# Kernel tuning notes

Measured on AMD Instinct MI355X. Metric: run time of the kernel, lower is better.

Reference implementation:

```python
import jax, jax.numpy as jnp
import numpy as np

B, D, N, H = 2, 512, 2048, 8
DK = D // H
EPS = 1e-5


def conv1x1(x, w, b):
    # kernel-size-1 Conv1d == channel-mixing GEMM: (o,i) x (b,i,n) -> (b,o,n)
    return jnp.einsum('oi,bin->bon', w, x) + b[None, :, None]


def setup_inputs() -> dict:
    key = jax.random.key(0)
    ks = jax.random.split(key, 20)
    s = 0.02
    return {
        'init_query': jax.random.normal(ks[0], (B, D, N), jnp.float32),
        'key_t': jax.random.normal(ks[1], (B, D, N), jnp.float32),
        'value': jax.random.normal(ks[2], (B, D, N), jnp.float32),
        'mask': jax.random.randint(ks[3], (B, 1, N, N), 0, 2, jnp.int32),
        'Wq': jax.random.normal(ks[4], (D, D), jnp.float32) * s,
        'bq': jax.random.normal(ks[5], (D,), jnp.float32) * s,
        'Wk': jax.random.normal(ks[6], (D, D), jnp.float32) * s,
        'bk': jax.random.normal(ks[7], (D,), jnp.float32) * s,
        'Wv': jax.random.normal(ks[8], (D, D), jnp.float32) * s,
        'bv': jax.random.normal(ks[9], (D,), jnp.float32) * s,
        'Wm': jax.random.normal(ks[10], (D, D), jnp.float32) * s,
        'bm': jax.random.normal(ks[11], (D,), jnp.float32) * s,
        'W1': jax.random.normal(ks[12], (2 * D, 2 * D), jnp.float32) * s,
        'b1': jax.random.normal(ks[13], (2 * D,), jnp.float32) * s,
        'gamma': jnp.ones((2 * D,), jnp.float32),
        'beta': jnp.zeros((2 * D,), jnp.float32),
        'rmean': jax.random.normal(ks[14], (2 * D,), jnp.float32) * s,
        'rvar': jnp.abs(jax.random.normal(ks[15], (2 * D,), jnp.float32)) * 0.1 + 0.5,
        'W2': jax.random.normal(ks[16], (D, 2 * D), jnp.float32) * s,
        'b2': jnp.zeros((D,), jnp.float32),  # nn.init.constant_(bias, 0.0)
    }


def reference(init_query, key_t, value, mask, Wq, bq, Wk, bk, Wv, bv, Wm, bm,
              W1, b1, gamma, beta, rmean, rvar, W2, b2):
    # projections, split channels into (d_k, n_heads) exactly like torch .view
    q = conv1x1(init_query, Wq, bq).reshape(B, DK, H, N)
    k = conv1x1(key_t, Wk, bk).reshape(B, DK, H, N)
    v = conv1x1(value, Wv, bv).reshape(B, DK, H, N)
    scores = jnp.einsum('bdhn,bdhm->bhnm', q, k) / jnp.sqrt(jnp.float32(DK))
    scores = jnp.where(mask == 0, jnp.float32(-1e9), scores)
    attn = jax.nn.softmax(scores, axis=-1)
    x = jnp.einsum('bhnm,bdhm->bdhn', attn, v).reshape(B, D, N)
    x = conv1x1(x, Wm, bm)
    x = jnp.concatenate([x, init_query], axis=1)  # (B, 2D, N)
    h = conv1x1(x, W1, b1)
    # BatchNorm1d (inference mode with running stats) + ReLU
    h = (h - rmean[None, :, None]) * (gamma / jnp.sqrt(rvar + EPS))[None, :, None] + beta[None, :, None]
    h = jax.nn.relu(h)
    return conv1x1(h, W2, b2)
```

## Files before the change

### kernel.cpp

```cpp
#include <hip/hip_runtime.h>

typedef unsigned short u16;
typedef unsigned int u32;
typedef unsigned long long u64;
typedef long long i64;
typedef __bf16 bf16x8 __attribute__((ext_vector_type(8)));
typedef u16 u16x8 __attribute__((ext_vector_type(8)));
typedef float f32x4 __attribute__((ext_vector_type(4)));
typedef float f32x16 __attribute__((ext_vector_type(16)));

#define DEV __device__ __forceinline__

constexpr int BB = 2, DD = 512, NN = 2048, HH = 8, DKc = 64, D2 = 1024;

constexpr float QSC = 0.125f * 1.44269504088896340736f;

constexpr i64 MB = 1048576;
constexpr i64 OFF_CAT = 0;
constexpr i64 OFF_XKT = 8 * MB;
constexpr i64 OFF_XVT = 12 * MB;
constexpr i64 OFF_QH  = 16 * MB;
constexpr i64 OFF_KH  = 20 * MB;
constexpr i64 OFF_VT  = 24 * MB;
constexpr i64 OFF_HT  = 28 * MB;
constexpr i64 OFF_OP  = 36 * MB;
constexpr i64 OFF_LP  = 68 * MB;
constexpr i64 OFF_WQP = 69 * MB;
constexpr i64 OFF_WKP = 69 * MB + 524288;
constexpr i64 OFF_WVP = 69 * MB + 1048576;
constexpr i64 OFF_WMT = 69 * MB + 1572864;
constexpr i64 OFF_W1A = 71 * MB;
constexpr i64 OFF_W1C = 72 * MB;
constexpr i64 OFF_W2B = 74 * MB;
constexpr i64 OFF_BQP = 75 * MB;
constexpr i64 OFF_BKP = 75 * MB + 2048;
constexpr i64 OFF_BVP = 75 * MB + 4096;
constexpr i64 OFF_BNA = 75 * MB + 8192;
constexpr i64 OFF_BNC = 75 * MB + 12288;
constexpr i64 OFF_MSK = 76 * MB;

DEV u16 f2bf(float f) {
  u32 u = __float_as_uint(f);
  u = u + 0x7FFFu + ((u >> 16) & 1u);
  return (u16)(u >> 16);
}

DEV float bf2f(u16 u) { return __uint_as_float(((u32)u) << 16); }
DEV float bf2f32(u32 u) { return __uint_as_float(u << 16); }

DEV u32 packbf(float lo, float hi) {
  return __builtin_amdgcn_perm(__float_as_uint(hi), __float_as_uint(lo), 0x07060302u);
}

DEV float fexp2(float x) {
#if __has_builtin(__builtin_amdgcn_exp2f)
  return __builtin_amdgcn_exp2f(x);
#else
  return exp2f(x);
#endif
}

DEV bf16x8 ldfrag(const u16* p) {
  bf16x8 v;
  __builtin_memcpy(&v, __builtin_assume_aligned(p, 16), 16);
  return v;
}

DEV bf16x8 ldfrag2(const u16* p0, const u16* p1) {
  bf16x8 v;
  __builtin_memcpy(&v, __builtin_assume_aligned(p0, 8), 8);
  __builtin_memcpy((char*)&v + 8, __builtin_assume_aligned(p1, 8), 8);
  return v;
}

DEV bf16x8 ones8() {
  u16x8 u = {0x3F80, 0x3F80, 0x3F80, 0x3F80, 0x3F80, 0x3F80, 0x3F80, 0x3F80};
  bf16x8 v;
  __builtin_memcpy(&v, &u, 16);
  return v;
}

DEV void gload16(const void* g, void* lds) {
  __builtin_amdgcn_global_load_lds((__attribute__((address_space(1))) void*)g,
                                   (__attribute__((address_space(3))) void*)lds, 16, 0, 0);
}

DEV f32x4 mfma16(bf16x8 a, bf16x8 b, f32x4 c) {
  return __builtin_amdgcn_mfma_f32_16x16x32_bf16(a, b, c, 0, 0, 0);
}

DEV f32x16 mfma32(bf16x8 a, bf16x8 b, f32x16 c) {
  return __builtin_amdgcn_mfma_f32_32x32x16_bf16(a, b, c, 0, 0, 0);
}

__global__ __launch_bounds__(256) void prep_all(
    const float* __restrict__ Wq, const float* __restrict__ Wk, const float* __restrict__ Wv,
    const float* __restrict__ Wm, const float* __restrict__ W1, const float* __restrict__ W2,
    const float* __restrict__ bq, const float* __restrict__ bk, const float* __restrict__ bv,
    const float* __restrict__ bm, const float* __restrict__ b1, const float* __restrict__ gamma_,
    const float* __restrict__ beta_, const float* __restrict__ rmean,
    const float* __restrict__ rvar, const int* __restrict__ mask,
    const float* __restrict__ iq, const float* __restrict__ kt, const float* __restrict__ vv,
    u16* __restrict__ wqp, u16* __restrict__ wkp, u16* __restrict__ wvp, u16* __restrict__ wmt,
    u16* __restrict__ w1a, u16* __restrict__ w1c, u16* __restrict__ w2b,
    float* __restrict__ bqp, float* __restrict__ bkp, float* __restrict__ bvp,
    float* __restrict__ bna, float* __restrict__ bnc, u32* __restrict__ mw,
    u16* __restrict__ cat, u16* __restrict__ xkt, u16* __restrict__ xvt) {
  __shared__ float tile[32][33];
  const int blk = blockIdx.x, t = threadIdx.x;
  if (blk < 768) {
    const int which = blk >> 8, lb = blk & 255;
    const float* W = which == 0 ? Wq : (which == 1 ? Wk : Wv);
    u16* dst = which == 0 ? wqp : (which == 1 ? wkp : wvp);
    for (int e = lb * 256 + t; e < 262144; e += 65536) {
      int op = e >> 9, i = e & 511;
      int dk = op & 63, h = op >> 6;
      dst[e] = f2bf(W[(dk * 8 + h) * 512 + i]);
    }
  } else if (blk < 1024) {
    const int lb = blk - 768;
    for (int e = lb * 256 + t; e < 262144; e += 65536) {
      int cp = e >> 9, o = e & 511;
      int dk = cp & 63, h = cp >> 6;
      wmt[e] = f2bf(Wm[o * 512 + dk * 8 + h]);
    }
  } else if (blk < 1280) {
    const int lb = blk - 1024;
    for (int e = lb * 256 + t; e < 524288; e += 65536) {
      int row = e >> 9, o = e & 511;
      w1a[e] = f2bf(W1[(i64)row * 1024 + o]);
    }
  } else if (blk < 1536) {
    const int lb = blk - 1280;
    for (int e = lb * 256 + t; e < 524288; e += 65536) {
      int row = e >> 9, j = e & 511;
      w1c[(i64)row * 1024 + 512 + j] = f2bf(W1[(i64)row * 1024 + 512 + j]);
    }
  } else if (blk < 1792) {
    const int lb = blk - 1536;
    for (int e = lb * 256 + t; e < 524288; e += 65536) w2b[e] = f2bf(W2[e]);
  } else if (blk < 1808) {
    __shared__ float sm[4][64];
    const int base = (blk - 1792) * 64;
    const int el = t & 63, oq = t >> 6;
    const float* wrow = W1 + (i64)(base + el) * 1024 + oq * 128;
    const float* bmq = bm + oq * 128;
    float s = 0.f;
#pragma unroll 8
    for (int j = 0; j < 128; j += 4) {
      float4 x = *(const float4*)(wrow + j);
      float4 y = *(const float4*)(bmq + j);
      s += x.x * y.x + x.y * y.y + x.z * y.z + x.w * y.w;
    }
    sm[oq][el] = s;
    __syncthreads();
    if (t < 64) {
      int e = base + t;
      float a = gamma_[e] * rsqrtf(rvar[e] + 1e-5f);
      bna[e] = a;
      bnc[e] = (b1[e] - rmean[e]) * a + beta_[e] + a * (sm[0][t] + sm[1][t] + sm[2][t] + sm[3][t]);
    }
  } else if (blk == 1808) {
    for (int e = t; e < 512; e += 256) {
      int src = (e & 63) * 8 + (e >> 6);
      bqp[e] = bq[src]; bkp[e] = bk[src]; bvp[e] = bv[src];
    }
  } else if (blk < 2833) {
    const int tid = (blk - 1809) * 256 + t;
    const i64 base = (i64)tid * 32;
    const int4* mp = (const int4*)(mask + base);
    u32 word = 0;
#pragma unroll
    for (int j = 0; j < 8; ++j) {
      int4 x = mp[j];
      u32 nib = (x.x != 0 ? 1u : 0u) | (x.y != 0 ? 2u : 0u) | (x.z != 0 ? 4u : 0u) |
                (x.w != 0 ? 8u : 0u);
      word |= nib << (j * 4);
    }
    mw[tid] = word;
  } else {
    const int idx = blk - 2833;
    const int bx = idx & 63, by = (idx >> 6) & 15, bz = idx >> 10;
    const int tensor = bz >> 1, b = bz & 1;
    const float* src = (tensor == 0 ? iq : (tensor == 1 ? kt : vv)) + (i64)b * DD * NN;
    u16* dst; i64 ldd; int coff;
    if (tensor == 0)      { dst = cat + (i64)b * NN * D2; ldd = D2; coff = DD; }
    else if (tensor == 1) { dst = xkt + (i64)b * NN * DD; ldd = DD; coff = 0; }
    else                  { dst = xvt + (i64)b * NN * DD; ldd = DD; coff = 0; }
    const int x0 = bx * 32, y0 = by * 32;
    const int col = t & 31, rg = t >> 5;
#pragma unroll
    for (int i = 0; i < 4; ++i) {
      int row = rg + i * 8;
      tile[row][col] = src[(i64)(y0 + row) * NN + x0 + col];
    }
    __syncthreads();
    const int dp = t & 15, rbase = t >> 4;
    u32* dst32 = (u32*)dst;
    const i64 ldw = ldd >> 1;
    const int cw = (coff + y0) >> 1;
#pragma unroll
    for (int i = 0; i < 2; ++i) {
      int rr = rbase + i * 16;
      dst32[(i64)(x0 + rr) * ldw + cw + dp] = packbf(tile[2 * dp][rr], tile[2 * dp + 1][rr]);
    }
  }
}

template <int AM, int AN>
DEV void gemm_core(const u16* __restrict__ A, i64 lda, const u16* __restrict__ Bp, i64 ldb,
                   int K, u16* As, u16* Bs, f32x4 (&acc)[AM][AN]) {
  constexpr int BM = AM * 32, BN = AN * 32;
  const int t = threadIdx.x, w = t >> 6, l = t & 63, quad = l >> 4, l15 = l & 15;
  const int wm = (w >> 1) * AM * 16, wn = (w & 1) * AN * 16;
  auto stage = [&](int kk, int buf) {
    u16* Ad = As + buf * (BM * 64);
    u16* Bd = Bs + buf * (BN * 64);
#pragma unroll
    for (int j = 0; j < BM / 32; ++j) {
      int ch = j * 256 + w * 64 + l, r = ch >> 3, c = ch & 7;
      gload16(A + (i64)r * lda + kk + ((c ^ (r & 7)) << 3), Ad + (j * 256 + w * 64) * 8);
    }
#pragma unroll
    for (int j = 0; j < BN / 32; ++j) {
      int ch = j * 256 + w * 64 + l, r = ch >> 3, c = ch & 7;
      gload16(Bp + (i64)r * ldb + kk + ((c ^ (r & 7)) << 3), Bd + (j * 256 + w * 64) * 8);
    }
  };
  const int nst = K >> 6;
  stage(0, 0);
  asm volatile("s_waitcnt vmcnt(0)" ::: "memory");
  __builtin_amdgcn_s_barrier();
  for (int s = 0; s < nst; ++s) {
    if (s + 1 < nst) stage((s + 1) << 6, (s + 1) & 1);
    const u16* Ac = As + (s & 1) * (BM * 64);
    const u16* Bc = Bs + (s & 1) * (BN * 64);
#pragma unroll
    for (int kc = 0; kc < 2; ++kc) {
      const int sw = ((kc * 4 + quad) ^ (l15 & 7)) << 3;
      bf16x8 af[AM], bfr[AN];
#pragma unroll
      for (int i = 0; i < AM; ++i) af[i] = ldfrag(&Ac[(wm + i * 16 + l15) * 64 + sw]);
#pragma unroll
      for (int j = 0; j < AN; ++j) bfr[j] = ldfrag(&Bc[(wn + j * 16 + l15) * 64 + sw]);
#pragma unroll
      for (int i = 0; i < AM; ++i)
#pragma unroll
        for (int j = 0; j < AN; ++j) acc[i][j] = mfma16(af[i], bfr[j], acc[i][j]);
    }
    asm volatile("s_waitcnt vmcnt(0) lgkmcnt(0)" ::: "memory");
    __builtin_amdgcn_s_barrier();
  }
}

__global__ __launch_bounds__(256) void qkv_gemm(const u16* __restrict__ cat,
                                                const u16* __restrict__ xkt,
                                                const u16* __restrict__ xvt,
                                                const u16* __restrict__ wqp,
                                                const u16* __restrict__ wkp,
                                                const u16* __restrict__ wvp,
                                                const u16* __restrict__ w1a,
                                                const u16* __restrict__ wmt,
                                                const float* __restrict__ bqp,
                                                const float* __restrict__ bkp,
                                                const float* __restrict__ bvp,
                                                u16* __restrict__ qh, u16* __restrict__ kh,
                                                u16* __restrict__ vt, u16* __restrict__ w1c) {
  __shared__ __align__(16) u16 As[2 * 128 * 64];
  __shared__ __align__(16) u16 Bs[2 * 128 * 64];
  const int flat = blockIdx.x;
  const int t = threadIdx.x, w = t >> 6, l = t & 63, quad = l >> 4, l15 = l & 15;
  const int wm = (w >> 1) * 64, wn = (w & 1) * 64;
  int op, b = 0, mx, ny;
  if (flat < 256) {
    op = flat >> 7;
    b = (flat >> 6) & 1;
    const int r = flat & 63;
    mx = r >> 2; ny = r & 3;
  } else if (flat < 384) {
    op = 2;
    const int r = flat - 256;
    b = r >> 6;
    const int rr = r & 63;
    mx = rr >> 4; ny = rr & 15;
  } else {
    op = 3;
    const int r = flat - 384;
    mx = r >> 2; ny = r & 3;
  }
  const u16 *A, *Bp;
  i64 lda, ldb;
  if (op < 2) {
    A = (op == 0 ? cat + DD : xkt);
    lda = (op == 0 ? D2 : DD);
    A += (i64)b * NN * lda + (i64)mx * 128 * lda;
    Bp = (op == 0 ? wqp : wkp) + (i64)ny * 128 * DD;
    ldb = DD;
  } else if (op == 2) {
    A = wvp + (i64)mx * 128 * DD; lda = DD;
    Bp = xvt + (i64)b * NN * DD + (i64)ny * 128 * DD; ldb = DD;
  } else {
    A = w1a + (i64)mx * 128 * DD; lda = DD;
    Bp = wmt + (i64)ny * 128 * DD; ldb = DD;
  }
  f32x4 acc[4][4] = {};
  gemm_core<4, 4>(A, lda, Bp, ldb, DD, As, Bs, acc);

  const int rowBase = mx * 128 + wm + quad * 4;
  const int colBase = ny * 128 + wn + l15;
  if (op < 2) {
    const float* bias = (op == 0 ? bqp : bkp);
    const float sc = (op == 0 ? QSC : 1.f);
    u16* dst = (op == 0 ? qh : kh) + (i64)b * HH * NN * DKc;
#pragma unroll
    for (int j = 0; j < 4; ++j) {
      const int col = colBase + j * 16;
      const float cA = bias[col];
#pragma unroll
      for (int i = 0; i < 4; ++i)
#pragma unroll
        for (int r = 0; r < 4; ++r) {
          const int row = rowBase + i * 16 + r;
          dst[(i64)(col >> 6) * (NN * 64) + (i64)row * 64 + (col & 63)] =
              f2bf((acc[i][j][r] + cA) * sc);
        }
    }
  } else if (op == 2) {
    u16* dst = vt + (i64)b * HH * DKc * NN;
#pragma unroll
    for (int j = 0; j < 4; ++j) {
      const int col = colBase + j * 16;
#pragma unroll
      for (int i = 0; i < 4; ++i)
#pragma unroll
        for (int r = 0; r < 4; ++r) {
          const int row = rowBase + i * 16 + r;
          dst[(i64)row * NN + col] = f2bf(acc[i][j][r] + bvp[row]);
        }
    }
  } else {
#pragma unroll
    for (int j = 0; j < 4; ++j) {
      const int col = colBase + j * 16;
#pragma unroll
      for (int i = 0; i < 4; ++i)
#pragma unroll
        for (int r = 0; r < 4; ++r) {
          const int row = rowBase + i * 16 + r;
          w1c[(i64)row * D2 + col] = f2bf(acc[i][j][r]);
        }
    }
  }
}

struct GArgs {
  const u16* A; i64 lda, sAb;
  const u16* B; i64 ldb, sBb;
  void* C; i64 ldc, sCb;
  const float* p1; const float* p2;
  int K;
};

template <int MODE, int AM, int AN, int SWZ>
__global__ __launch_bounds__(256) void gemm_bt(GArgs g) {
  __shared__ __align__(16) u16 As[2 * AM * 32 * 64];
  __shared__ __align__(16) u16 Bs[2 * AN * 32 * 64];
  const int t = threadIdx.x, w = t >> 6, l = t & 63, quad = l >> 4, l15 = l & 15;
  const int wm = (w >> 1) * AM * 16, wn = (w & 1) * AN * 16;
  int bx = blockIdx.x, by = blockIdx.y, bz = blockIdx.z;
  if (SWZ == 1) {
    const int i = bx + (by << 3) + (bz << 8);
    const int slot = i & 7, jj = i >> 3;
    by = slot + ((jj & 3) << 3);
    const int j2 = jj >> 2;
    bx = j2 & 7;
    bz = j2 >> 3;
  }
  const u16* A = g.A + (i64)bz * g.sAb + (i64)bx * (AM * 32) * g.lda;
  const u16* Bp = g.B + (i64)bz * g.sBb + (i64)by * (AN * 32) * g.ldb;
  f32x4 acc[AM][AN] = {};
  gemm_core<AM, AN>(A, g.lda, Bp, g.ldb, g.K, As, Bs, acc);

  const int rowBase = bx * (AM * 32) + wm + quad * 4;
  const int colBase = by * (AN * 32) + wn + l15;
#pragma unroll
  for (int j = 0; j < AN; ++j) {
    const int col = colBase + j * 16;
    float cA = 0.f, cB = 0.f;
    if (MODE == 3) { cA = g.p1[col]; cB = g.p2[col]; }
#pragma unroll
    for (int i = 0; i < AM; ++i) {
#pragma unroll
      for (int r = 0; r < 4; ++r) {
        const int row = rowBase + i * 16 + r;
        float v = acc[i][j][r];
        if (MODE == 3) {
          float x = v * cA + cB;
          ((u16*)g.C + (i64)bz * g.sCb)[(i64)row * g.ldc + col] = f2bf(x > 0.f ? x : 0.f);
        } else {
          ((float*)g.C + (i64)bz * g.sCb)[(i64)row * g.ldc + col] = v + g.p1[row];
        }
      }
    }
  }
}

__global__ __launch_bounds__(512) void flash_attn(const u16* __restrict__ Qh,
                                                  const u16* __restrict__ Kh,
                                                  const u16* __restrict__ Vt,
                                                  const u64* __restrict__ MW64,
                                                  u16* __restrict__ Opart,
                                                  float* __restrict__ Lp) {
  __shared__ __align__(16) u16 Ks0[64 * 64];
  __shared__ __align__(16) u16 Ks1[64 * 64];
  __shared__ __align__(16) u16 Vs0[64 * 64];
  __shared__ __align__(16) u16 Vs1[64 * 64];
  const int t = threadIdx.x, w = t >> 6, l = t & 63, l31 = l & 31, lh = l >> 5;
  const int flat = blockIdx.x;
  const int h = flat & 7;
  const int j = flat >> 3;
  const int nt = j & 7, zz = j >> 3;
  const int sp = zz & 1, b = zz >> 1;
  const int n = nt * 256 + w * 32 + l31;
  const u16* Qb = Qh + ((i64)(b * HH + h) * NN + nt * 256 + w * 32) * 64;
  const u16* Kb = Kh + (i64)(b * HH + h) * NN * 64;
  const u16* Vb = Vt + (i64)(b * HH + h) * 64 * NN;
  const u64* mwp = MW64 + (i64)(b * NN + n) * 32;
  const bf16x8 ONE = ones8();
  bf16x8 qf[4];
#pragma unroll
  for (int kc = 0; kc < 4; ++kc)
    __builtin_memcpy(&qf[kc], Qb + (i64)l31 * 64 + kc * 16 + lh * 8, 16);

  f32x16 oacc0 = {}, oacc1 = {}, lacc = {};
  const int mt0 = sp * 16;

  auto stage = [&](u16* Kd, u16* Vd, int mt) {
    const int r = t >> 3, c = t & 7;
    gload16(Kb + (i64)(mt * 64 + r) * 64 + ((c ^ (r & 7)) << 3), Kd + t * 8);
    gload16(Vb + (i64)r * NN + mt * 64 + ((c ^ (r & 7)) << 3), Vd + t * 8);
  };
  auto compute = [&](const u16* Kc, const u16* Vc, int mt) {
    f32x16 s0 = {}, s1 = {};
    __builtin_amdgcn_s_setprio(1);
#pragma unroll
    for (int kc = 0; kc < 4; ++kc) {
      const int sw = l31 & 7;
      bf16x8 k0 = ldfrag(&Kc[l31 * 64 + (((kc * 2 + lh) ^ sw) << 3)]);
      bf16x8 k1 = ldfrag(&Kc[(32 + l31) * 64 + (((kc * 2 + lh) ^ sw) << 3)]);
      s0 = mfma32(k0, qf[kc], s0);
      s1 = mfma32(k1, qf[kc], s1);
    }
    __builtin_amdgcn_s_setprio(0);
    const u64 mrow = mwp[mt];
    u32 pw[16];
#pragma unroll
    for (int k = 0; k < 8; ++k) {
      const int kvb = ((2 * k) & 3) + 8 * ((2 * k) >> 2) + 4 * lh;
      u64 sh = mrow >> kvb;
      u32 mA = (((u32)sh & 1u) | (((u32)sh & 2u) << 15)) * 0xFFFFu;
      u32 shh = (u32)(sh >> 32);
      u32 mB = ((shh & 1u) | ((shh & 2u) << 15)) * 0xFFFFu;
      pw[k] = packbf(fexp2(s0[2 * k]), fexp2(s0[2 * k + 1])) & mA;
      pw[8 + k] = packbf(fexp2(s1[2 * k]), fexp2(s1[2 * k + 1])) & mB;
    }
    bf16x8 pf[4];
#pragma unroll
    for (int c = 0; c < 4; ++c) __builtin_memcpy(&pf[c], &pw[c * 4], 16);
    __builtin_amdgcn_s_setprio(1);
#pragma unroll
    for (int c = 0; c < 4; ++c) lacc = mfma32(ONE, pf[c], lacc);
#pragma unroll
    for (int c = 0; c < 4; ++c) {
      const int sw0 = l31 & 7;
      const u16* r0 = &Vc[l31 * 64];
      const u16* r1 = &Vc[(32 + l31) * 64];
      bf16x8 v0 = ldfrag2(r0 + (((2 * c) ^ sw0) << 3) + lh * 4,
                          r0 + (((2 * c + 1) ^ sw0) << 3) + lh * 4);
      bf16x8 v1 = ldfrag2(r1 + (((2 * c) ^ sw0) << 3) + lh * 4,
                          r1 + (((2 * c + 1) ^ sw0) << 3) + lh * 4);
      oacc0 = mfma32(v0, pf[c], oacc0);
      oacc1 = mfma32(v1, pf[c], oacc1);
    }
    __builtin_amdgcn_s_setprio(0);
  };

  stage(Ks0, Vs0, mt0);
  for (int ii = 0; ii < 8; ++ii) {
    const int m = mt0 + 2 * ii;
    __syncthreads();
    stage(Ks1, Vs1, m + 1);
    compute(Ks0, Vs0, m);
    __syncthreads();
    if (ii < 7) stage(Ks0, Vs0, m + 2);
    compute(Ks1, Vs1, m + 1);
  }
  u16* OpT = Opart + ((i64)((sp * BB + b) * HH + h) * 64) * NN;
#pragma unroll
  for (int r = 0; r < 16; ++r) {
    const int d0 = (r & 3) + 8 * (r >> 2) + 4 * lh;
    OpT[(i64)d0 * NN + n] = f2bf(oacc0[r]);
    OpT[(i64)(d0 + 32) * NN + n] = f2bf(oacc1[r]);
  }
  if (lh == 0) Lp[((i64)(sp * BB + b) * HH + h) * NN + n] = lacc[0];
}

__global__ __launch_bounds__(256) void combine(const u16* __restrict__ Opart,
                                               const float* __restrict__ Lp,
                                               u16* __restrict__ cat) {
  __shared__ float lt[128 * 65];
  const int t = threadIdx.x;
  const int nt = blockIdx.x, bh = blockIdx.y;
  const int b = bh >> 3, h = bh & 7;
  const int n0 = nt * 128;
  const i64 sstride = (i64)BB * HH * 64 * NN;
  const u16* Ob = Opart + ((i64)(b * HH + h) * 64) * NN;
#pragma unroll
  for (int i = 0; i < 16; ++i) {
    const int idx = i * 256 + t;
    const int d = idx >> 6, np = idx & 63;
    float sa = 0.f, sb = 0.f;
#pragma unroll
    for (int s = 0; s < 2; ++s) {
      u32 v;
      __builtin_memcpy(&v, Ob + s * sstride + (i64)d * NN + n0 + 2 * np, 4);
      sa += bf2f32(v & 0xFFFFu);
      sb += bf2f32(v >> 16);
    }
    lt[(2 * np) * 65 + d] = sa;
    lt[(2 * np + 1) * 65 + d] = sb;
  }
  __syncthreads();
  u32* catw = (u32*)cat;
#pragma unroll
  for (int i = 0; i < 16; ++i) {
    const int idx = i * 256 + t;
    const int nn = idx >> 5, dp = idx & 31;
    float lsum = 0.f;
#pragma unroll
    for (int s = 0; s < 2; ++s) lsum += Lp[((i64)(s * BB + b) * HH + h) * NN + n0 + nn];
    const float rl = __builtin_amdgcn_rcpf(lsum);
    u32 pv = packbf(lt[nn * 65 + 2 * dp] * rl, lt[nn * 65 + 2 * dp + 1] * rl);
    catw[((i64)b * NN + n0 + nn) * (D2 / 2) + h * 32 + dp] = pv;
  }
}

extern "C" void kernel_launch(void* const* d_in, const int* in_sizes, int n_in,
                              void* d_out, int out_size, void* d_ws, size_t ws_size,
                              hipStream_t stream) {
  (void)in_sizes; (void)n_in; (void)out_size; (void)ws_size;
  const float* iq    = (const float*)d_in[0];
  const float* kt    = (const float*)d_in[1];
  const float* vv    = (const float*)d_in[2];
  const int*   mask  = (const int*)d_in[3];
  const float* Wq    = (const float*)d_in[4];
  const float* bq    = (const float*)d_in[5];
  const float* Wk    = (const float*)d_in[6];
  const float* bk    = (const float*)d_in[7];
  const float* Wv    = (const float*)d_in[8];
  const float* bv    = (const float*)d_in[9];
  const float* Wm    = (const float*)d_in[10];
  const float* bm    = (const float*)d_in[11];
  const float* W1    = (const float*)d_in[12];
  const float* b1    = (const float*)d_in[13];
  const float* gamma_= (const float*)d_in[14];
  const float* beta_ = (const float*)d_in[15];
  const float* rmean = (const float*)d_in[16];
  const float* rvar  = (const float*)d_in[17];
  const float* W2    = (const float*)d_in[18];
  const float* b2    = (const float*)d_in[19];

  char* ws = (char*)d_ws;
  u16* cat = (u16*)(ws + OFF_CAT);
  u16* xkt = (u16*)(ws + OFF_XKT);
  u16* xvt = (u16*)(ws + OFF_XVT);
  u16* qh  = (u16*)(ws + OFF_QH);
  u16* kh  = (u16*)(ws + OFF_KH);
  u16* vt  = (u16*)(ws + OFF_VT);
  u16* ht  = (u16*)(ws + OFF_HT);
  u16* opart = (u16*)(ws + OFF_OP);
  float* lp  = (float*)(ws + OFF_LP);
  u16* wqp = (u16*)(ws + OFF_WQP);
  u16* wkp = (u16*)(ws + OFF_WKP);
  u16* wvp = (u16*)(ws + OFF_WVP);
  u16* wmt = (u16*)(ws + OFF_WMT);
  u16* w1a = (u16*)(ws + OFF_W1A);
  u16* w1c = (u16*)(ws + OFF_W1C);
  u16* w2b = (u16*)(ws + OFF_W2B);
  float* bqp = (float*)(ws + OFF_BQP);
  float* bkp = (float*)(ws + OFF_BKP);
  float* bvp = (float*)(ws + OFF_BVP);
  float* bna = (float*)(ws + OFF_BNA);
  float* bnc = (float*)(ws + OFF_BNC);
  u32* mw = (u32*)(ws + OFF_MSK);

  prep_all<<<8977, 256, 0, stream>>>(Wq, Wk, Wv, Wm, W1, W2, bq, bk, bv, bm, b1, gamma_, beta_,
                                     rmean, rvar, mask, iq, kt, vv, wqp, wkp, wvp, wmt, w1a, w1c,
                                     w2b, bqp, bkp, bvp, bna, bnc, mw, cat, xkt, xvt);
  qkv_gemm<<<416, 256, 0, stream>>>(cat, xkt, xvt, wqp, wkp, wvp, w1a, wmt,
                                    bqp, bkp, bvp, qh, kh, vt, w1c);
  flash_attn<<<256, 512, 0, stream>>>(qh, kh, vt, (const u64*)mw, opart, lp);
  combine<<<dim3(16, 16), 256, 0, stream>>>(opart, lp, cat);
  GArgs wa{cat, D2, 0, w1c, D2, 0, ht, D2, 0, bna, bnc, D2};
  gemm_bt<3, 4, 2, 0><<<dim3(32, 16, 1), 256, 0, stream>>>(wa);
  GArgs w2a{w2b, D2, 0, ht, D2, (i64)NN * D2, d_out, NN, (i64)DD * NN, b2, nullptr, D2};
  gemm_bt<4, 2, 2, 1><<<dim3(8, 32, 2), 256, 0, stream>>>(w2a);
}
```

Before: 211.7 us.

## Fuse split-K attention combine into flash kernel via atomic last-block flag

Removes the separate combine kernel. Each flash-attention block writes its partial output and row sums, then bumps a per-(batch, head, tile) atomic counter. The second block to arrive reads the partner's partial, adds its own register accumulators, normalises, and writes the concatenated bf16 output through LDS. This saves a kernel launch and one read of the partials, but adds atomics, fences and an imbalanced tail where only half the blocks do the combine.

```diff
diff --git a/kernel.cpp b/kernel.cpp
--- a/kernel.cpp
+++ b/kernel.cpp
@@ -25,6 +25,7 @@
 constexpr i64 OFF_HT  = 28 * MB;
 constexpr i64 OFF_OP  = 36 * MB;
 constexpr i64 OFF_LP  = 68 * MB;
+constexpr i64 OFF_FLG = 68 * MB + 524288;
 constexpr i64 OFF_WQP = 69 * MB;
 constexpr i64 OFF_WKP = 69 * MB + 524288;
 constexpr i64 OFF_WVP = 69 * MB + 1048576;
@@ -105,6 +106,7 @@
     u16* __restrict__ w1a, u16* __restrict__ w1c, u16* __restrict__ w2b,
     float* __restrict__ bqp, float* __restrict__ bkp, float* __restrict__ bvp,
     float* __restrict__ bna, float* __restrict__ bnc, u32* __restrict__ mw,
+    u32* __restrict__ flg,
     u16* __restrict__ cat, u16* __restrict__ xkt, u16* __restrict__ xvt) {
   __shared__ float tile[32][33];
   const int blk = blockIdx.x, t = threadIdx.x;
@@ -165,6 +167,7 @@
       int src = (e & 63) * 8 + (e >> 6);
       bqp[e] = bq[src]; bkp[e] = bk[src]; bvp[e] = bv[src];
     }
+    if (t < 128) flg[t] = 0u;
   } else if (blk < 2833) {
     const int tid = (blk - 1809) * 256 + t;
     const i64 base = (i64)tid * 32;
@@ -410,18 +413,22 @@
                                                   const u16* __restrict__ Vt,
                                                   const u64* __restrict__ MW64,
                                                   u16* __restrict__ Opart,
-                                                  float* __restrict__ Lp) {
-  __shared__ __align__(16) u16 Ks0[64 * 64];
-  __shared__ __align__(16) u16 Ks1[64 * 64];
-  __shared__ __align__(16) u16 Vs0[64 * 64];
-  __shared__ __align__(16) u16 Vs1[64 * 64];
+                                                  float* __restrict__ Lp,
+                                                  u32* __restrict__ flags,
+                                                  u16* __restrict__ cat) {
+  __shared__ __align__(16) u16 smem[4 * 4096];
+  u16* Ks0 = smem;
+  u16* Ks1 = smem + 4096;
+  u16* Vs0 = smem + 8192;
+  u16* Vs1 = smem + 12288;
   const int t = threadIdx.x, w = t >> 6, l = t & 63, l31 = l & 31, lh = l >> 5;
   const int flat = blockIdx.x;
   const int h = flat & 7;
   const int j = flat >> 3;
   const int nt = j & 7, zz = j >> 3;
   const int sp = zz & 1, b = zz >> 1;
-  const int n = nt * 256 + w * 32 + l31;
+  const int nl = w * 32 + l31;
+  const int n = nt * 256 + nl;
   const u16* Qb = Qh + ((i64)(b * HH + h) * NN + nt * 256 + w * 32) * 64;
   const u16* Kb = Kh + (i64)(b * HH + h) * NN * 64;
   const u16* Vb = Vt + (i64)(b * HH + h) * 64 * NN;
@@ -495,6 +502,7 @@
     if (ii < 7) stage(Ks0, Vs0, m + 2);
     compute(Ks1, Vs1, m + 1);
   }
+
   u16* OpT = Opart + ((i64)((sp * BB + b) * HH + h) * 64) * NN;
 #pragma unroll
   for (int r = 0; r < 16; ++r) {
@@ -503,45 +511,43 @@
     OpT[(i64)(d0 + 32) * NN + n] = f2bf(oacc1[r]);
   }
   if (lh == 0) Lp[((i64)(sp * BB + b) * HH + h) * NN + n] = lacc[0];
-}
-
-__global__ __launch_bounds__(256) void combine(const u16* __restrict__ Opart,
-                                               const float* __restrict__ Lp,
-                                               u16* __restrict__ cat) {
-  __shared__ float lt[128 * 65];
-  const int t = threadIdx.x;
-  const int nt = blockIdx.x, bh = blockIdx.y;
-  const int b = bh >> 3, h = bh & 7;
-  const int n0 = nt * 128;
-  const i64 sstride = (i64)BB * HH * 64 * NN;
-  const u16* Ob = Opart + ((i64)(b * HH + h) * 64) * NN;
-#pragma unroll
-  for (int i = 0; i < 16; ++i) {
-    const int idx = i * 256 + t;
-    const int d = idx >> 6, np = idx & 63;
-    float sa = 0.f, sb = 0.f;
-#pragma unroll
-    for (int s = 0; s < 2; ++s) {
-      u32 v;
-      __builtin_memcpy(&v, Ob + s * sstride + (i64)d * NN + n0 + 2 * np, 4);
-      sa += bf2f32(v & 0xFFFFu);
-      sb += bf2f32(v >> 16);
-    }
-    lt[(2 * np) * 65 + d] = sa;
-    lt[(2 * np + 1) * 65 + d] = sb;
-  }
+
+  __shared__ u32 sflag;
   __syncthreads();
-  u32* catw = (u32*)cat;
-#pragma unroll
-  for (int i = 0; i < 16; ++i) {
-    const int idx = i * 256 + t;
-    const int nn = idx >> 5, dp = idx & 31;
-    float lsum = 0.f;
-#pragma unroll
-    for (int s = 0; s < 2; ++s) lsum += Lp[((i64)(s * BB + b) * HH + h) * NN + n0 + nn];
+  if (t == 0) {
+    __builtin_amdgcn_fence(__ATOMIC_RELEASE, "agent");
+    const int pair = ((b * HH + h) << 3) | nt;
+    sflag = atomicAdd(&flags[pair], 1u);
+  }
+  __syncthreads();
+  if (sflag == 1u) {
+    __builtin_amdgcn_fence(__ATOMIC_ACQUIRE, "agent");
+    const int spo = sp ^ 1;
+    const u16* OpP = Opart + ((i64)((spo * BB + b) * HH + h) * 64) * NN;
+    const float lsum = lacc[0] + Lp[((i64)(spo * BB + b) * HH + h) * NN + n];
     const float rl = __builtin_amdgcn_rcpf(lsum);
-    u32 pv = packbf(lt[nn * 65 + 2 * dp] * rl, lt[nn * 65 + 2 * dp + 1] * rl);
-    catw[((i64)b * NN + n0 + nn) * (D2 / 2) + h * 32 + dp] = pv;
+    u32* lds32 = (u32*)smem;
+#pragma unroll
+    for (int e = 0; e < 8; ++e) {
+      const int r0 = 2 * e, r1 = 2 * e + 1;
+      const int d0 = (r0 & 3) + 8 * (r0 >> 2) + 4 * lh;
+      const float a0 = oacc0[r0] + bf2f(OpP[(i64)d0 * NN + n]);
+      const float a1 = oacc0[r1] + bf2f(OpP[(i64)(d0 + 1) * NN + n]);
+      const float b0 = oacc1[r0] + bf2f(OpP[(i64)(d0 + 32) * NN + n]);
+      const float b1 = oacc1[r1] + bf2f(OpP[(i64)(d0 + 33) * NN + n]);
+      const int dp0 = d0 >> 1;
+      lds32[nl * 32 + (dp0 ^ (nl & 31))] = packbf(a0 * rl, a1 * rl);
+      lds32[nl * 32 + ((dp0 + 16) ^ (nl & 31))] = packbf(b0 * rl, b1 * rl);
+    }
+    __syncthreads();
+    u32* catw = (u32*)cat;
+#pragma unroll
+    for (int i = 0; i < 16; ++i) {
+      const int idx = i * 512 + t;
+      const int nn = idx >> 5, dp = idx & 31;
+      const u32 v = lds32[nn * 32 + (dp ^ (nn & 31))];
+      catw[((i64)b * NN + nt * 256 + nn) * (D2 / 2) + h * 32 + dp] = v;
+    }
   }
 }
 
@@ -580,6 +586,7 @@
   u16* ht  = (u16*)(ws + OFF_HT);
   u16* opart = (u16*)(ws + OFF_OP);
   float* lp  = (float*)(ws + OFF_LP);
+  u32* flags = (u32*)(ws + OFF_FLG);
   u16* wqp = (u16*)(ws + OFF_WQP);
   u16* wkp = (u16*)(ws + OFF_WKP);
   u16* wvp = (u16*)(ws + OFF_WVP);
@@ -596,11 +603,10 @@
 
   prep_all<<<8977, 256, 0, stream>>>(Wq, Wk, Wv, Wm, W1, W2, bq, bk, bv, bm, b1, gamma_, beta_,
                                      rmean, rvar, mask, iq, kt, vv, wqp, wkp, wvp, wmt, w1a, w1c,
-                                     w2b, bqp, bkp, bvp, bna, bnc, mw, cat, xkt, xvt);
+                                     w2b, bqp, bkp, bvp, bna, bnc, mw, flags, cat, xkt, xvt);
   qkv_gemm<<<416, 256, 0, stream>>>(cat, xkt, xvt, wqp, wkp, wvp, w1a, wmt,
                                     bqp, bkp, bvp, qh, kh, vt, w1c);
-  flash_attn<<<256, 512, 0, stream>>>(qh, kh, vt, (const u64*)mw, opart, lp);
-  combine<<<dim3(16, 16), 256, 0, stream>>>(opart, lp, cat);
+  flash_attn<<<256, 512, 0, stream>>>(qh, kh, vt, (const u64*)mw, opart, lp, flags, cat);
   GArgs wa{cat, D2, 0, w1c, D2, 0, ht, D2, 0, bna, bnc, D2};
   gemm_bt<3, 4, 2, 0><<<dim3(32, 16, 1), 256, 0, stream>>>(wa);
   GArgs w2a{w2b, D2, 0, ht, D2, (i64)NN * D2, d_out, NN, (i64)DD * NN, b2, nullptr, D2};
```

Result: slower. 226.2 us (+6.9%).

## Deepen flash-attention K/V pipeline to four LDS slots with prefetch distance two

Applied to the files above, without the earlier changes.

Replaces the double-buffered K/V staging in the attention kernel with a four-slot ring buffer, keeping two tiles in flight and using explicit vmcnt waits plus one barrier per tile instead of two __syncthreads. All sixteen mask words are also preloaded into registers up front, taking the mask load off the per-tile critical path. The aim is to hide global-load latency and halve the barrier count per tile. The costs are twice the LDS per block (64 KB), which may lower occupancy, and extra register pressure from the mask array and full unrolling.

```diff
diff --git a/kernel.cpp b/kernel.cpp
--- a/kernel.cpp
+++ b/kernel.cpp
@@ -411,10 +411,7 @@
                                                   const u64* __restrict__ MW64,
                                                   u16* __restrict__ Opart,
                                                   float* __restrict__ Lp) {
-  __shared__ __align__(16) u16 Ks0[64 * 64];
-  __shared__ __align__(16) u16 Ks1[64 * 64];
-  __shared__ __align__(16) u16 Vs0[64 * 64];
-  __shared__ __align__(16) u16 Vs1[64 * 64];
+  __shared__ __align__(16) u16 smem[4 * 8192];
   const int t = threadIdx.x, w = t >> 6, l = t & 63, l31 = l & 31, lh = l >> 5;
   const int flat = blockIdx.x;
   const int h = flat & 7;
@@ -427,20 +424,27 @@
   const u16* Vb = Vt + (i64)(b * HH + h) * 64 * NN;
   const u64* mwp = MW64 + (i64)(b * NN + n) * 32;
   const bf16x8 ONE = ones8();
+  const int mt0 = sp * 16;
+
+  u64 mrows[16];
+#pragma unroll
+  for (int m = 0; m < 16; ++m) mrows[m] = mwp[mt0 + m];
   bf16x8 qf[4];
 #pragma unroll
   for (int kc = 0; kc < 4; ++kc)
     __builtin_memcpy(&qf[kc], Qb + (i64)l31 * 64 + kc * 16 + lh * 8, 16);
 
   f32x16 oacc0 = {}, oacc1 = {}, lacc = {};
-  const int mt0 = sp * 16;
-
-  auto stage = [&](u16* Kd, u16* Vd, int mt) {
+
+  auto stage = [&](int slot, int mt) {
+    u16* Kd = smem + slot * 8192;
     const int r = t >> 3, c = t & 7;
     gload16(Kb + (i64)(mt * 64 + r) * 64 + ((c ^ (r & 7)) << 3), Kd + t * 8);
-    gload16(Vb + (i64)r * NN + mt * 64 + ((c ^ (r & 7)) << 3), Vd + t * 8);
+    gload16(Vb + (i64)r * NN + mt * 64 + ((c ^ (r & 7)) << 3), Kd + 4096 + t * 8);
   };
-  auto compute = [&](const u16* Kc, const u16* Vc, int mt) {
+  auto compute = [&](int slot, u64 mrow) {
+    const u16* Kc = smem + slot * 8192;
+    const u16* Vc = Kc + 4096;
     f32x16 s0 = {}, s1 = {};
     __builtin_amdgcn_s_setprio(1);
 #pragma unroll
@@ -452,7 +456,6 @@
       s1 = mfma32(k1, qf[kc], s1);
     }
     __builtin_amdgcn_s_setprio(0);
-    const u64 mrow = mwp[mt];
     u32 pw[16];
 #pragma unroll
     for (int k = 0; k < 8; ++k) {
@@ -485,16 +488,19 @@
     __builtin_amdgcn_s_setprio(0);
   };
 
-  stage(Ks0, Vs0, mt0);
-  for (int ii = 0; ii < 8; ++ii) {
-    const int m = mt0 + 2 * ii;
-    __syncthreads();
-    stage(Ks1, Vs1, m + 1);
-    compute(Ks0, Vs0, m);
-    __syncthreads();
-    if (ii < 7) stage(Ks0, Vs0, m + 2);
-    compute(Ks1, Vs1, m + 1);
-  }
+  stage(0, mt0);
+  stage(1, mt0 + 1);
+#pragma unroll
+  for (int i = 0; i < 15; ++i) {
+    asm volatile("s_waitcnt vmcnt(2)" ::: "memory");
+    __builtin_amdgcn_s_barrier();
+    if (i + 2 < 16) stage((i + 2) & 3, mt0 + i + 2);
+    compute(i & 3, mrows[i]);
+  }
+  asm volatile("s_waitcnt vmcnt(0)" ::: "memory");
+  __builtin_amdgcn_s_barrier();
+  compute(15 & 3, mrows[15]);
+
   u16* OpT = Opart + ((i64)((sp * BB + b) * HH + h) * 64) * NN;
 #pragma unroll
   for (int r = 0; r < 16; ++r) {
```

After: 214.1 us. About the same (+1.1%).

## Store K and V projections in pre-tiled LDS-ready layout for attention

Applied to the files above, without the earlier changes.

The K and V projection epilogues now write their bf16 outputs in a blocked layout of 64-row tiles with 8-element column groups, matching the order the attention kernel wants in LDS. Staging becomes a contiguous 16-byte copy per thread, and the LDS fragment reads drop the XOR swizzle arithmetic. This aims to coalesce the global loads in attention and cut index math. The trade-off is scattered stores in the GEMM epilogue and possible LDS bank conflicts, since the swizzle is gone.

```diff
diff --git a/kernel.cpp b/kernel.cpp
--- a/kernel.cpp
+++ b/kernel.cpp
@@ -308,21 +308,36 @@
 
   const int rowBase = mx * 128 + wm + quad * 4;
   const int colBase = ny * 128 + wn + l15;
-  if (op < 2) {
-    const float* bias = (op == 0 ? bqp : bkp);
-    const float sc = (op == 0 ? QSC : 1.f);
-    u16* dst = (op == 0 ? qh : kh) + (i64)b * HH * NN * DKc;
+  if (op == 0) {
+    u16* dst = qh + (i64)b * HH * NN * DKc;
 #pragma unroll
     for (int j = 0; j < 4; ++j) {
       const int col = colBase + j * 16;
-      const float cA = bias[col];
+      const float cA = bqp[col];
 #pragma unroll
       for (int i = 0; i < 4; ++i)
 #pragma unroll
         for (int r = 0; r < 4; ++r) {
           const int row = rowBase + i * 16 + r;
           dst[(i64)(col >> 6) * (NN * 64) + (i64)row * 64 + (col & 63)] =
-              f2bf((acc[i][j][r] + cA) * sc);
+              f2bf((acc[i][j][r] + cA) * QSC);
+        }
+    }
+  } else if (op == 1) {
+    u16* dst = kh + (i64)b * HH * NN * DKc;
+#pragma unroll
+    for (int j = 0; j < 4; ++j) {
+      const int col = colBase + j * 16;
+      const float cA = bkp[col];
+      const i64 hbase = (i64)(col >> 6) * (NN * 64);
+      const int g = (col >> 3) & 7, e = col & 7;
+#pragma unroll
+      for (int i = 0; i < 4; ++i)
+#pragma unroll
+        for (int r = 0; r < 4; ++r) {
+          const int row = rowBase + i * 16 + r;
+          dst[hbase + (i64)(row >> 6) * 4096 + g * 512 + (row & 63) * 8 + e] =
+              f2bf(acc[i][j][r] + cA);
         }
     }
   } else if (op == 2) {
@@ -330,12 +345,14 @@
 #pragma unroll
     for (int j = 0; j < 4; ++j) {
       const int col = colBase + j * 16;
+      const i64 tbase = (i64)(col >> 6) * 4096 + ((col >> 3) & 7) * 512 + (col & 7);
 #pragma unroll
       for (int i = 0; i < 4; ++i)
 #pragma unroll
         for (int r = 0; r < 4; ++r) {
           const int row = rowBase + i * 16 + r;
-          dst[(i64)row * NN + col] = f2bf(acc[i][j][r] + bvp[row]);
+          dst[(i64)(row >> 6) * (DKc * NN) + tbase + (row & 63) * 8] =
+              f2bf(acc[i][j][r] + bvp[row]);
         }
     }
   } else {
@@ -424,7 +441,7 @@
   const int n = nt * 256 + w * 32 + l31;
   const u16* Qb = Qh + ((i64)(b * HH + h) * NN + nt * 256 + w * 32) * 64;
   const u16* Kb = Kh + (i64)(b * HH + h) * NN * 64;
-  const u16* Vb = Vt + (i64)(b * HH + h) * 64 * NN;
+  const u16* Vb = Vt + (i64)(b * HH + h) * DKc * NN;
   const u64* mwp = MW64 + (i64)(b * NN + n) * 32;
   const bf16x8 ONE = ones8();
   bf16x8 qf[4];
@@ -436,18 +453,16 @@
   const int mt0 = sp * 16;
 
   auto stage = [&](u16* Kd, u16* Vd, int mt) {
-    const int r = t >> 3, c = t & 7;
-    gload16(Kb + (i64)(mt * 64 + r) * 64 + ((c ^ (r & 7)) << 3), Kd + t * 8);
-    gload16(Vb + (i64)r * NN + mt * 64 + ((c ^ (r & 7)) << 3), Vd + t * 8);
+    gload16(Kb + (i64)mt * 4096 + t * 8, Kd + t * 8);
+    gload16(Vb + (i64)mt * 4096 + t * 8, Vd + t * 8);
   };
   auto compute = [&](const u16* Kc, const u16* Vc, int mt) {
     f32x16 s0 = {}, s1 = {};
     __builtin_amdgcn_s_setprio(1);
 #pragma unroll
     for (int kc = 0; kc < 4; ++kc) {
-      const int sw = l31 & 7;
-      bf16x8 k0 = ldfrag(&Kc[l31 * 64 + (((kc * 2 + lh) ^ sw) << 3)]);
-      bf16x8 k1 = ldfrag(&Kc[(32 + l31) * 64 + (((kc * 2 + lh) ^ sw) << 3)]);
+      bf16x8 k0 = ldfrag(&Kc[(kc * 2 + lh) * 512 + l31 * 8]);
+      bf16x8 k1 = ldfrag(&Kc[(kc * 2 + lh) * 512 + (32 + l31) * 8]);
       s0 = mfma32(k0, qf[kc], s0);
       s1 = mfma32(k1, qf[kc], s1);
     }
@@ -472,13 +487,10 @@
     for (int c = 0; c < 4; ++c) lacc = mfma32(ONE, pf[c], lacc);
 #pragma unroll
     for (int c = 0; c < 4; ++c) {
-      const int sw0 = l31 & 7;
-      const u16* r0 = &Vc[l31 * 64];
-      const u16* r1 = &Vc[(32 + l31) * 64];
-      bf16x8 v0 = ldfrag2(r0 + (((2 * c) ^ sw0) << 3) + lh * 4,
-                          r0 + (((2 * c + 1) ^ sw0) << 3) + lh * 4);
-      bf16x8 v1 = ldfrag2(r1 + (((2 * c) ^ sw0) << 3) + lh * 4,
-                          r1 + (((2 * c + 1) ^ sw0) << 3) + lh * 4);
+      bf16x8 v0 = ldfrag2(&Vc[(2 * c) * 512 + l31 * 8 + lh * 4],
+                          &Vc[(2 * c + 1) * 512 + l31 * 8 + lh * 4]);
+      bf16x8 v1 = ldfrag2(&Vc[(2 * c) * 512 + (32 + l31) * 8 + lh * 4],
+                          &Vc[(2 * c + 1) * 512 + (32 + l31) * 8 + lh * 4]);
       oacc0 = mfma32(v0, pf[c], oacc0);
       oacc1 = mfma32(v1, pf[c], oacc1);
     }
```

Measured after the change: 220.8 us. +4.3%, slower.
